# Kernel optimization log

Measured on AMD Instinct MI355X. Metric: run time of the kernel, lower is better.

The kernel has to match this reference:

```python
import jax, jax.numpy as jnp
import numpy as np

GROUPS = 4      # DySample groups (default)
DSTATE = 16     # SSM state size
BN_EPS = 1e-5


def grid_sample_border(img, grid):
    # img: (N, C, H, W); grid: (N, Ho, Wo, 2), xy order, [-1, 1], align_corners=False,
    # padding_mode='border' (coords clamped before bilinear interp).
    N, C, H, W = img.shape
    x = jnp.clip((grid[..., 0] + 1.0) * (W * 0.5) - 0.5, 0.0, W - 1.0)
    y = jnp.clip((grid[..., 1] + 1.0) * (H * 0.5) - 0.5, 0.0, H - 1.0)
    x0 = jnp.floor(x); y0 = jnp.floor(y)
    wx = (x - x0)[:, None]; wy = (y - y0)[:, None]          # (N,1,Ho,Wo)
    x0i = x0.astype(jnp.int32); y0i = y0.astype(jnp.int32)
    x1i = jnp.minimum(x0i + 1, W - 1); y1i = jnp.minimum(y0i + 1, H - 1)
    gat = jax.vmap(lambda im, yy, xx: im[:, yy, xx])        # (C,H,W),(Ho,Wo)->(C,Ho,Wo)
    v00 = gat(img, y0i, x0i); v01 = gat(img, y0i, x1i)
    v10 = gat(img, y1i, x0i); v11 = gat(img, y1i, x1i)
    return v00 * (1 - wx) * (1 - wy) + v01 * wx * (1 - wy) + v10 * (1 - wx) * wy + v11 * wx * wy


def dysample(x, off_w, off_b, scale):
    # DySample 'lp' style (ICCV'23), groups=4, no dyscope.
    B, C, H, W = x.shape
    s, g = scale, GROUPS
    conv = jnp.einsum('bchw,co->bohw', x, off_w) + off_b[None, :, None, None]  # (B, 2*g*s*s, H, W)
    hh = ((jnp.arange(s) - (s - 1) / 2.0) / s).astype(x.dtype)                 # subpixel init positions
    ip_x = jnp.broadcast_to(hh[None, None, :], (g, s, s))
    ip_y = jnp.broadcast_to(hh[None, :, None], (g, s, s))
    ip = jnp.stack([ip_x, ip_y])                                               # (2, g, s, s)
    off = conv.reshape(B, 2, g, s, s, H, W) * 0.25 + ip[None, :, :, :, :, None, None]
    cx = jnp.arange(W, dtype=x.dtype) + 0.5
    cy = jnp.arange(H, dtype=x.dtype) + 0.5
    gx = 2.0 * (cx + off[:, 0]) / W - 1.0                                      # (B,g,s,s,H,W)
    gy = 2.0 * (cy[:, None] + off[:, 1]) / H - 1.0
    # pixel_shuffle: (B,g,si,sj,H,W) -> (B,g,H,si,W,sj) -> (B,g,sH,sW)
    gx = gx.transpose(0, 1, 4, 2, 5, 3).reshape(B, g, s * H, s * W)
    gy = gy.transpose(0, 1, 4, 2, 5, 3).reshape(B, g, s * H, s * W)
    grid = jnp.stack([gx, gy], -1).reshape(B * g, s * H, s * W, 2)
    xg = x.reshape(B * g, C // g, H, W)
    return grid_sample_border(xg, grid).reshape(B, C, s * H, s * W)


def channel_ssm(x, in_w, in_b, xproj_w, dt_w, dt_b, A_log, Dp, out_w, out_b):
    # Channel-wise bidirectional selective scan (S6) over the channel axis, gating x.
    B, C, H, W = x.shape
    n = DSTATE
    s = x.mean((-2, -1))                            # (B, C) channel descriptor
    u = s[..., None] * in_w + in_b                  # (B, C, d)
    proj = u @ xproj_w                              # (B, C, 1 + 2n)
    dt_raw = proj[..., :1]
    Bs = proj[..., 1:1 + n]
    Cs = proj[..., 1 + n:]
    dt = jax.nn.softplus(dt_raw * dt_w + dt_b)      # (B, C, d)
    A = -jnp.exp(A_log)                             # (d, n)
    dA = jnp.exp(dt[..., None] * A)                 # (B, C, d, n)
    dBu = (dt * u)[..., None] * Bs[:, :, None, :]   # (B, C, d, n)

    def scan_dir(dA_, dBu_, Cs_):
        def step(h, inp):
            a, b, c = inp
            h = a * h + b                           # (B, d, n)
            return h, jnp.einsum('bdn,bn->bd', h, c)
        h0 = jnp.zeros((B, dA_.shape[2], n), x.dtype)
        _, ys = jax.lax.scan(step, h0, (jnp.swapaxes(dA_, 0, 1), jnp.swapaxes(dBu_, 0, 1), jnp.swapaxes(Cs_, 0, 1)))
        return jnp.swapaxes(ys, 0, 1)               # (B, C, d)

    y = scan_dir(dA, dBu, Cs)
    y = y + scan_dir(dA[:, ::-1], dBu[:, ::-1], Cs[:, ::-1])[:, ::-1]
    y = y + Dp * u
    gate = jax.nn.sigmoid(y @ out_w + out_b)        # (B, C)
    return x * gate[:, :, None, None]


def setup_inputs():
    key = jax.random.key(0)
    ks = jax.random.split(key, 24)
    f = jnp.float32
    rn = lambda k, shp, sc=1.0: jax.random.normal(k, shp, dtype=f) * sc
    B = 2
    inp = {}
    inp['c1'] = rn(ks[0], (B, 96, 128, 128))
    inp['c2'] = rn(ks[1], (B, 96, 64, 64))
    inp['c3'] = rn(ks[2], (B, 192, 32, 32))
    inp['c4'] = rn(ks[3], (B, 384, 16, 16))
    inp['mlp1_w'] = rn(ks[4], (96, 384), 0.05); inp['mlp1_b'] = jnp.zeros((384,), f)
    inp['mlp2_w'] = rn(ks[5], (96, 384), 0.05); inp['mlp2_b'] = jnp.zeros((384,), f)
    inp['mlp3_w'] = rn(ks[6], (192, 384), 0.05); inp['mlp3_b'] = jnp.zeros((384,), f)
    inp['mlp4_w'] = rn(ks[7], (384, 384), 0.05); inp['mlp4_b'] = jnp.zeros((384,), f)
    inp['up2_w'] = rn(ks[8], (384, 2 * 4 * 4), 0.001); inp['up2_b'] = jnp.zeros((2 * 4 * 4,), f)
    inp['up4_w'] = rn(ks[9], (384, 2 * 4 * 16), 0.001); inp['up4_b'] = jnp.zeros((2 * 4 * 16,), f)
    inp['up8_w'] = rn(ks[10], (384, 2 * 4 * 64), 0.001); inp['up8_b'] = jnp.zeros((2 * 4 * 64,), f)
    inp['ssm_in_w'] = rn(ks[11], (64,), 0.5); inp['ssm_in_b'] = rn(ks[12], (64,), 0.1)
    inp['ssm_xproj_w'] = rn(ks[13], (64, 1 + 2 * 16), 0.1)
    inp['ssm_dt_w'] = rn(ks[14], (64,), 0.1); inp['ssm_dt_b'] = jnp.full((64,), -2.0, f)
    inp['ssm_A_log'] = jnp.log(jnp.broadcast_to(jnp.arange(1, 17, dtype=f), (64, 16)))
    inp['ssm_D'] = jnp.ones((64,), f)
    inp['ssm_out_w'] = rn(ks[15], (64,), 0.1); inp['ssm_out_b'] = jnp.zeros((), f)
    inp['fuse_w'] = rn(ks[16], (1536, 384), 0.02)
    inp['bn_g'] = jnp.ones((384,), f); inp['bn_b'] = jnp.zeros((384,), f)
    inp['bn_m'] = jnp.zeros((384,), f); inp['bn_v'] = jnp.ones((384,), f)
    inp['pred_w'] = rn(ks[17], (384, 6), 0.05); inp['pred_b'] = jnp.zeros((6,), f)
    inp['bird_w'] = rn(ks[18], (384, 2), 0.05); inp['bird_b'] = jnp.zeros((2,), f)
    return inp


def reference(c1, c2, c3, c4, mlp1_w, mlp1_b, mlp2_w, mlp2_b, mlp3_w, mlp3_b, mlp4_w, mlp4_b,
              up2_w, up2_b, up4_w, up4_b, up8_w, up8_b,
              ssm_in_w, ssm_in_b, ssm_xproj_w, ssm_dt_w, ssm_dt_b, ssm_A_log, ssm_D, ssm_out_w, ssm_out_b,
              fuse_w, bn_g, bn_b, bn_m, bn_v, pred_w, pred_b, bird_w, bird_b):
    proj = lambda c, w, b: jnp.einsum('bchw,ce->behw', c, w) + b[None, :, None, None]
    _c4 = dysample(proj(c4, mlp4_w, mlp4_b), up8_w, up8_b, 8)
    _c3 = dysample(proj(c3, mlp3_w, mlp3_b), up4_w, up4_b, 4)
    _c2 = dysample(proj(c2, mlp2_w, mlp2_b), up2_w, up2_b, 2)
    _c1 = proj(c1, mlp1_w, mlp1_b)
    cc = jnp.concatenate([_c4, _c3, _c2, _c1], axis=1)      # (B, 1536, 128, 128)
    cc = channel_ssm(cc, ssm_in_w, ssm_in_b, ssm_xproj_w, ssm_dt_w, ssm_dt_b, ssm_A_log, ssm_D, ssm_out_w, ssm_out_b)
    h = jnp.einsum('bchw,co->bohw', cc, fuse_w)             # 1x1 conv, no bias
    h = (h - bn_m[None, :, None, None]) * (bn_g / jnp.sqrt(bn_v + BN_EPS))[None, :, None, None] + bn_b[None, :, None, None]
    h = jax.nn.relu(h)                                      # dropout = identity (eval)
    out = jnp.einsum('bchw,co->bohw', h, pred_w) + pred_b[None, :, None, None]
    aux = jnp.einsum('bchw,co->bohw', h, bird_w) + bird_b[None, :, None, None]
    return (out, aux)
```

## Files before the change

kernel.cpp:

```cpp
#include <hip/hip_runtime.h>
#include <cstddef>

#define HWO 16384
#define CTOT 1536

typedef __attribute__((ext_vector_type(8))) short bf16x8;
typedef __attribute__((ext_vector_type(4))) float f32x4;

__device__ inline unsigned short f2bf(float x) {
  union { float f; unsigned u; } v; v.f = x;
  unsigned r = v.u + 0x7FFFu + ((v.u >> 16) & 1u);
  return (unsigned short)(r >> 16);
}
__device__ inline float bf2f(unsigned short h) {
  union { unsigned u; float f; } v; v.u = ((unsigned)h) << 16; return v.f;
}

struct __align__(16) Prm { unsigned short i00, i01, i10, i11; float wx, wy; };

struct SetupArgs {
  const float* W[7];
  unsigned short* T[7];
  int K[7], N[7], bstart[8];
  const float *bn_g, *bn_v, *bn_m, *bn_b;
  float *sc, *sh;
  const float* c1;
  float* mc1;
  const float* fw;
  unsigned short* fwt;
  int nTP;
};
__global__ __launch_bounds__(256) void setup_kernel(SetupArgs a) {
  int bid = blockIdx.x;
  if (bid < a.nTP) {
    int s = 0;
#pragma unroll
    for (int i = 1; i < 7; i++) if (bid >= a.bstart[i]) s = i;
    const int K = a.K[s], N = a.N[s];
    const int idx = (bid - a.bstart[s]) * 256 + threadIdx.x;
    if (idx >= K * N) return;
    const int k = idx / N, o = idx - k * N;
    a.T[s][(size_t)o * K + k] = f2bf(a.W[s][idx]);
    return;
  }
  bid -= a.nTP;
  if (bid < 2) {
    const int o = bid * 256 + threadIdx.x;
    if (o < 384) {
      const float sc = a.bn_g[o] * rsqrtf(a.bn_v[o] + 1e-5f);
      a.sc[o] = sc;
      a.sh[o] = a.bn_b[o] - a.bn_m[o] * sc;
    }
    return;
  }
  bid -= 2;
  if (bid < 192) {
    const float4* p = (const float4*)(a.c1 + (size_t)bid * HWO);
    float acc = 0.f;
    for (int i = threadIdx.x; i < HWO / 4; i += 256) {
      const float4 v = p[i];
      acc += (v.x + v.y) + (v.z + v.w);
    }
    for (int o = 32; o > 0; o >>= 1) acc += __shfl_down(acc, o, 64);
    __shared__ float red[4];
    if ((threadIdx.x & 63) == 0) red[threadIdx.x >> 6] = acc;
    __syncthreads();
    if (threadIdx.x == 0)
      a.mc1[bid] = (red[0] + red[1] + red[2] + red[3]) * (1.0f / HWO);
    return;
  }
  bid -= 192;
  const int tk = bid / 12, to = bid % 12;
  __shared__ float tile[32][33];
  const int rr0 = threadIdx.x >> 5, cch = threadIdx.x & 31;
#pragma unroll
  for (int rr = rr0; rr < 32; rr += 8)
    tile[rr][cch] = a.fw[(size_t)(tk * 32 + rr) * 384 + to * 32 + cch];
  __syncthreads();
#pragma unroll
  for (int rr = rr0; rr < 32; rr += 8)
    a.fwt[(size_t)(to * 32 + rr) * 1536 + tk * 32 + cch] = f2bf(tile[cch][rr]);
}

struct PSeg { const float* X; const unsigned short* Wt; const float* bias;
              unsigned short* Y; int P, K, blk0; };
struct PArgs { PSeg s[4]; };
__global__ __launch_bounds__(256) void proj_all(PArgs a) {
  int si = 0;
#pragma unroll
  for (int i = 1; i < 4; i++) if ((int)blockIdx.x >= a.s[i].blk0) si = i;
  const PSeg sg = a.s[si];
  const int rel = blockIdx.x - sg.blk0;
  const int pb = rel >> 1, ob = rel & 1;
  const int b = blockIdx.y;
  const int P = sg.P, K = sg.K;
  const int p0 = pb * 128;
  constexpr int LST = 40;
  __shared__ unsigned short Alds[128 * LST];
  __shared__ unsigned short Blds[192 * LST];
  const int tid = threadIdx.x;
  const int w = tid >> 6, lane = tid & 63;
  const int wm = w >> 1, wn = w & 1;
  const float* Xf = sg.X + (long)b * K * P;
  const unsigned short* Wt = sg.Wt;
  f32x4 acc[24];
#pragma unroll
  for (int i = 0; i < 24; i++) acc[i] = (f32x4){0.f, 0.f, 0.f, 0.f};
  const int lr = lane & 15, lk = (lane >> 4) * 8;

  for (int kc = 0; kc < K; kc += 32) {
#pragma unroll
    for (int it = 0; it < 4; it++) {
      const int idx = tid + it * 256;
      const int k = idx >> 5, pg = (idx & 31) * 4;
      const float4 v = *(const float4*)(Xf + (long)(kc + k) * P + p0 + pg);
      Alds[(pg + 0) * LST + k] = f2bf(v.x);
      Alds[(pg + 1) * LST + k] = f2bf(v.y);
      Alds[(pg + 2) * LST + k] = f2bf(v.z);
      Alds[(pg + 3) * LST + k] = f2bf(v.w);
    }
#pragma unroll
    for (int it = 0; it < 3; it++) {
      const int idx = tid + it * 256;
      const int r = idx >> 2, ck = (idx & 3) * 8;
      *(uint4*)&Blds[r * LST + ck] =
          *(const uint4*)(Wt + (long)(ob * 192 + r) * K + kc + ck);
    }
    __syncthreads();
    bf16x8 af[4];
#pragma unroll
    for (int mt = 0; mt < 4; mt++)
      af[mt] = *(const bf16x8*)&Alds[((wm * 4 + mt) * 16 + lr) * LST + lk];
#pragma unroll
    for (int ot = 0; ot < 6; ot++) {
      const bf16x8 bfr = *(const bf16x8*)&Blds[((wn * 6 + ot) * 16 + lr) * LST + lk];
#pragma unroll
      for (int mt = 0; mt < 4; mt++)
        acc[mt * 6 + ot] = __builtin_amdgcn_mfma_f32_16x16x32_bf16(
            af[mt], bfr, acc[mt * 6 + ot], 0, 0, 0);
    }
    __syncthreads();
  }
  const int r0 = (lane >> 4) * 4;
#pragma unroll
  for (int mt = 0; mt < 4; mt++) {
#pragma unroll
    for (int ot = 0; ot < 6; ot++) {
      const int o = ob * 192 + (wn * 6 + ot) * 16 + lr;
      const float bv = sg.bias[o];
      const f32x4 r = acc[mt * 6 + ot];
#pragma unroll
      for (int jj = 0; jj < 4; jj++) {
        const long row = p0 + (wm * 4 + mt) * 16 + r0 + jj;
        sg.Y[((long)b * P + row) * 384 + o] = f2bf(r[jj] + bv);
      }
    }
  }
}

struct OSeg { const unsigned short* X; const unsigned short* Wt;
              const float* bias; float* Y; int P, N, obn, blk0; };
struct OArgs { OSeg s[3]; };
__global__ __launch_bounds__(256) void offs_all(OArgs a) {
  int si = 0;
#pragma unroll
  for (int i = 1; i < 3; i++) if ((int)blockIdx.x >= a.s[i].blk0) si = i;
  const OSeg sg = a.s[si];
  const int rel = blockIdx.x - sg.blk0;
  const int pb = rel / sg.obn, ob = rel - pb * sg.obn;
  const int b = blockIdx.y;
  const int P = sg.P, N = sg.N;
  const int p0 = pb * 128, o0 = ob * 128;
  constexpr int LST = 40;
  __shared__ unsigned short Alds[128 * LST];
  __shared__ unsigned short Blds[128 * LST];
  const int tid = threadIdx.x;
  const int w = tid >> 6, lane = tid & 63;
  const int wm = w >> 1, wn = w & 1;
  const unsigned short* Xb = sg.X + (long)b * P * 384;
  f32x4 acc[16];
#pragma unroll
  for (int i = 0; i < 16; i++) acc[i] = (f32x4){0.f, 0.f, 0.f, 0.f};
  const int lr = lane & 15, lk = (lane >> 4) * 8;

  for (int kc = 0; kc < 384; kc += 32) {
#pragma unroll
    for (int it = 0; it < 2; it++) {
      const int idx = tid + it * 256;
      const int r = idx >> 2, ck = (idx & 3) * 8;
      *(uint4*)&Alds[r * LST + ck] =
          *(const uint4*)(Xb + (long)(p0 + r) * 384 + kc + ck);
    }
#pragma unroll
    for (int it = 0; it < 2; it++) {
      const int idx = tid + it * 256;
      const int r = idx >> 2, ck = (idx & 3) * 8;
      uint4 v = {0u, 0u, 0u, 0u};
      if (o0 + r < N)
        v = *(const uint4*)(sg.Wt + (long)(o0 + r) * 384 + kc + ck);
      *(uint4*)&Blds[r * LST + ck] = v;
    }
    __syncthreads();
    bf16x8 af[4];
#pragma unroll
    for (int mt = 0; mt < 4; mt++)
      af[mt] = *(const bf16x8*)&Alds[((wm * 4 + mt) * 16 + lr) * LST + lk];
#pragma unroll
    for (int ot = 0; ot < 4; ot++) {
      const bf16x8 bfr = *(const bf16x8*)&Blds[((wn * 4 + ot) * 16 + lr) * LST + lk];
#pragma unroll
      for (int mt = 0; mt < 4; mt++)
        acc[mt * 4 + ot] = __builtin_amdgcn_mfma_f32_16x16x32_bf16(
            af[mt], bfr, acc[mt * 4 + ot], 0, 0, 0);
    }
    __syncthreads();
  }
  const int r0 = (lane >> 4) * 4;
#pragma unroll
  for (int mt = 0; mt < 4; mt++) {
#pragma unroll
    for (int ot = 0; ot < 4; ot++) {
      const int o = o0 + (wn * 4 + ot) * 16 + lr;
      if (o < N) {
        const float bv = sg.bias[o];
        const f32x4 r = acc[mt * 4 + ot];
#pragma unroll
        for (int jj = 0; jj < 4; jj++) {
          const long row = p0 + (wm * 4 + mt) * 16 + r0 + jj;
          sg.Y[((long)b * P + row) * N + o] = r[jj] + bv;
        }
      }
    }
  }
}

__global__ __launch_bounds__(256) void pm_kernel(
    const float* __restrict__ bo4, const float* __restrict__ bo3,
    const float* __restrict__ bo2,
    const unsigned short* __restrict__ bp4, const unsigned short* __restrict__ bp3,
    const unsigned short* __restrict__ bp2,
    Prm* __restrict__ prm, float* __restrict__ part) {
  const int gp = blockIdx.y, b = blockIdx.z;
  const int lvl = gp >> 2, g = gp & 3;
  const float* bo; int ls, H, offC;
  const unsigned short* bpL; int HWs_;
  if (lvl == 0)      { bo = bo4; ls = 3; H = 16; offC = 512; bpL = bp4; HWs_ = 256; }
  else if (lvl == 1) { bo = bo3; ls = 2; H = 32; offC = 128; bpL = bp3; HWs_ = 1024; }
  else               { bo = bo2; ls = 1; H = 64; offC = 32;  bpL = bp2; HWs_ = 4096; }
  const int s = 1 << ls, ss = s * s, W = H;
  const int tid = threadIdx.x;
  __shared__ Prm Plds[512];

#pragma unroll
  for (int ii = 0; ii < 2; ii++) {
    const int li = tid + ii * 256;
    const int p = blockIdx.x * 512 + li;
    const int yo = p >> 7, xo = p & 127;
    const int h = yo >> ls, i = yo & (s - 1);
    const int w = xo >> ls, j = xo & (s - 1);
    const int sp = h * W + w;
    const float* offp = bo + ((size_t)b * (W * H) + sp) * offC;
    const float cx = offp[g * ss + i * s + j];
    const float cy = offp[(4 + g) * ss + i * s + j];
    const float inv_s = 1.0f / (float)s;
    const float offx = cx * 0.25f + ((float)j - (s - 1) * 0.5f) * inv_s;
    const float offy = cy * 0.25f + ((float)i - (s - 1) * 0.5f) * inv_s;
    float xf = fminf(fmaxf((float)w + offx, 0.0f), (float)(W - 1));
    float yf = fminf(fmaxf((float)h + offy, 0.0f), (float)(H - 1));
    const float x0f = floorf(xf), y0f = floorf(yf);
    const int x0 = (int)x0f, y0 = (int)y0f;
    const int x1 = min(x0 + 1, W - 1), y1 = min(y0 + 1, H - 1);
    Prm pr;
    pr.i00 = (unsigned short)(y0 * W + x0);
    pr.i01 = (unsigned short)(y0 * W + x1);
    pr.i10 = (unsigned short)(y1 * W + x0);
    pr.i11 = (unsigned short)(y1 * W + x1);
    pr.wx = xf - x0f;
    pr.wy = yf - y0f;
    prm[((size_t)b * 12 + gp) * HWO + p] = pr;
    Plds[li] = pr;
  }
  __syncthreads();

  const int chunk = tid % 12, pl = tid / 12;
  float acc[8];
#pragma unroll
  for (int j = 0; j < 8; j++) acc[j] = 0.f;
  const unsigned short* qb = bpL + (size_t)b * HWs_ * 384 + g * 96 + chunk * 8;
  if (tid < 252) {
    for (int it = 0; it < 25; it++) {
      const int pli = it * 21 + pl;
      if (pli < 512) {
        const Prm pr = Plds[pli];
        const float wx = pr.wx, wy = pr.wy;
        const float w00 = (1.f - wx) * (1.f - wy), w01 = wx * (1.f - wy);
        const float w10 = (1.f - wx) * wy, w11 = wx * wy;
        const uint4 v00 = *(const uint4*)(qb + (size_t)pr.i00 * 384);
        const uint4 v01 = *(const uint4*)(qb + (size_t)pr.i01 * 384);
        const uint4 v10 = *(const uint4*)(qb + (size_t)pr.i10 * 384);
        const uint4 v11 = *(const uint4*)(qb + (size_t)pr.i11 * 384);
        const unsigned short* s00 = (const unsigned short*)&v00;
        const unsigned short* s01 = (const unsigned short*)&v01;
        const unsigned short* s10 = (const unsigned short*)&v10;
        const unsigned short* s11 = (const unsigned short*)&v11;
#pragma unroll
        for (int j = 0; j < 8; j++)
          acc[j] += w00 * bf2f(s00[j]) + w01 * bf2f(s01[j]) +
                    w10 * bf2f(s10[j]) + w11 * bf2f(s11[j]);
      }
    }
  }
  __shared__ float red[12][8][22];
  if (tid < 252) {
#pragma unroll
    for (int j = 0; j < 8; j++) red[chunk][j][pl] = acc[j];
  }
  __syncthreads();
  if (tid < 96) {
    float sum = 0.f;
#pragma unroll
    for (int l = 0; l < 21; l++) sum += red[tid >> 3][tid & 7][l];
    part[((size_t)blockIdx.x * 2 + b) * 1152 + gp * 96 + tid] = sum;
  }
}

__global__ __launch_bounds__(64) void ssm_prep(
    const float* __restrict__ part, const float* __restrict__ mc1,
    const float* __restrict__ mlp1_w, const float* __restrict__ mlp1_b,
    const float* __restrict__ in_w, const float* __restrict__ in_b,
    const float* __restrict__ xproj_w, const float* __restrict__ dt_w,
    const float* __restrict__ dt_b, float* __restrict__ u_out,
    float2* __restrict__ dtdu_out, float* __restrict__ Bs_out,
    float* __restrict__ Cs_out) {
  const int bc = blockIdx.x;
  const int b = bc / 1536, c = bc - b * 1536;
  const int d = threadIdx.x;
  float sv;
  if (c < 1152) {
    float a = (d < 32) ? part[((size_t)d * 2 + b) * 1152 + c] : 0.f;
    a += __shfl_xor(a, 1, 64);  a += __shfl_xor(a, 2, 64);
    a += __shfl_xor(a, 4, 64);  a += __shfl_xor(a, 8, 64);
    a += __shfl_xor(a, 16, 64); a += __shfl_xor(a, 32, 64);
    sv = a * (1.0f / HWO);
  } else {
    const int c2 = c - 1152;
    float a = mc1[b * 96 + d] * mlp1_w[d * 384 + c2];
    if (d < 32) a += mc1[b * 96 + 64 + d] * mlp1_w[(64 + d) * 384 + c2];
    a += __shfl_xor(a, 1, 64);  a += __shfl_xor(a, 2, 64);
    a += __shfl_xor(a, 4, 64);  a += __shfl_xor(a, 8, 64);
    a += __shfl_xor(a, 16, 64); a += __shfl_xor(a, 32, 64);
    sv = a + mlp1_b[c2];
  }
  const float u = sv * in_w[d] + in_b[d];
  __shared__ float ush[64];
  __shared__ float proj[33];
  ush[d] = u;
  __syncthreads();
  if (d < 33) {
    float acc = 0.f;
    for (int k = 0; k < 64; k++) acc = fmaf(ush[k], xproj_w[k * 33 + d], acc);
    proj[d] = acc;
  }
  __syncthreads();
  float dtv = proj[0] * dt_w[d] + dt_b[d];
  dtv = (dtv > 20.0f) ? dtv : log1pf(__expf(dtv));
  u_out[(size_t)bc * 64 + d] = u;
  dtdu_out[(size_t)bc * 64 + d] = make_float2(dtv, dtv * u);
  if (d < 16) {
    Bs_out[(size_t)bc * 16 + d] = proj[1 + d];
    Cs_out[(size_t)bc * 16 + d] = proj[17 + d];
  }
}

__global__ __launch_bounds__(256) void ssm_scan_par(
    const float2* __restrict__ dtdu, const float* __restrict__ Bs,
    const float* __restrict__ Cs, const float* __restrict__ A_log,
    float* __restrict__ y) {
  const int d = blockIdx.x, dir = blockIdx.y, b = blockIdx.z;
  const int t = threadIdx.x;
  const int j = t >> 4, n = t & 15;
  const float A = -__expf(A_log[d * 16 + n]);
  const int s0 = j * 96;
  const int c0 = dir ? (1535 - s0) : s0;
  const int step = dir ? -1 : 1;
  const float2* dbase = dtdu + (size_t)b * 1536 * 64 + (size_t)c0 * 64 + d;
  const float* bbase = Bs + (size_t)b * 1536 * 16 + (size_t)c0 * 16 + n;
  const float* cbase = Cs + (size_t)b * 1536 * 16 + (size_t)c0 * 16 + n;
  const long dstep = (long)step * 64;
  const long bstep = (long)step * 16;

  float Ap = 1.f, Bp = 0.f;
  {
    const float2* dp = dbase;
    const float* bp = bbase;
    float2 td = *dp;
    float Bv = *bp;
    for (int i = 0; i < 96; i++) {
      const float2 tdc = td;
      const float Bc = Bv;
      dp += dstep; bp += bstep;
      if (i + 1 < 96) { td = *dp; Bv = *bp; }
      const float a = __expf(tdc.x * A);
      Bp = fmaf(a, Bp, tdc.y * Bc);
      Ap *= a;
    }
  }
  __shared__ float sA[16][16], sB[16][16];
  sA[j][n] = Ap;
  sB[j][n] = Bp;
  __syncthreads();
  float H = 0.f;
  for (int jj = 0; jj < j; jj++) H = fmaf(sA[jj][n], H, sB[jj][n]);

  float* yb = y + (size_t)(b * 2 + dir) * 1536 * 64;
  {
    const float2* dp = dbase;
    const float* bp = bbase;
    const float* cp = cbase;
    float2 td = *dp;
    float Bv = *bp;
    float Cv = *cp;
    float h = H;
    int c = c0;
    for (int i = 0; i < 96; i++) {
      const float2 tdc = td;
      const float Bc = Bv, Cc = Cv;
      dp += dstep; bp += bstep; cp += bstep;
      if (i + 1 < 96) { td = *dp; Bv = *bp; Cv = *cp; }
      const float a = __expf(tdc.x * A);
      h = fmaf(a, h, tdc.y * Bc);
      float pr = h * Cc;
      pr += __shfl_xor(pr, 1, 64);
      pr += __shfl_xor(pr, 2, 64);
      pr += __shfl_xor(pr, 4, 64);
      pr += __shfl_xor(pr, 8, 64);
      if (n == 0) yb[(size_t)c * 64 + d] = pr;
      c += step;
    }
  }
}

__global__ __launch_bounds__(64) void gate_kernel(
    const float* __restrict__ y, const float* __restrict__ u,
    const float* __restrict__ Dp, const float* __restrict__ out_w,
    const float* __restrict__ out_b, float* __restrict__ gate) {
  const int c = blockIdx.x, b = blockIdx.y, d = threadIdx.x;
  const size_t i = ((size_t)b * 1536 + c) * 64 + d;
  float yt = y[((size_t)(b * 2) * 1536 + c) * 64 + d]
           + y[((size_t)(b * 2 + 1) * 1536 + c) * 64 + d]
           + Dp[d] * u[i];
  float v = yt * out_w[d];
  for (int o = 32; o > 0; o >>= 1) v += __shfl_down(v, o, 64);
  if (d == 0) gate[b * 1536 + c] = 1.0f / (1.0f + __expf(-(v + out_b[0])));
}

__global__ __launch_bounds__(256) void gate_fold(
    const unsigned short* __restrict__ wtf, const float* __restrict__ gate,
    unsigned short* __restrict__ wg) {
  const int b = blockIdx.y;
  const int idx8 = blockIdx.x * 256 + threadIdx.x;
  const int o = idx8 / 192;
  const int k0 = (idx8 - o * 192) * 8;
  const size_t idx = (size_t)o * 1536 + k0;
  const uint4 v = *(const uint4*)(wtf + idx);
  const unsigned short* s = (const unsigned short*)&v;
  const float* g = gate + b * 1536 + k0;
  unsigned short r8[8];
#pragma unroll
  for (int j = 0; j < 8; j++) r8[j] = f2bf(bf2f(s[j]) * g[j]);
  *(uint4*)(wg + (size_t)b * 589824 + idx) = *(const uint4*)r8;
}

__global__ __launch_bounds__(1024, 4) void fuse_gemm(
    const unsigned short* __restrict__ bp4, const unsigned short* __restrict__ bp3,
    const unsigned short* __restrict__ bp2, const unsigned short* __restrict__ bp1,
    const Prm* __restrict__ prm, const unsigned short* __restrict__ wg,
    const float* __restrict__ ep_a, const float* __restrict__ ep_b,
    unsigned short* __restrict__ hbf) {
  constexpr int LST = 40;
  __shared__ unsigned short Alds[128 * LST];
  __shared__ unsigned short Blds[384 * LST];
  const int tid = threadIdx.x;
  const int w = tid >> 6, lane = tid & 63;
  const int wm = w >> 2, wn = w & 3;
  const int b = blockIdx.y;
  const int p0 = blockIdx.x * 128;
  const unsigned short* Wb = wg + (size_t)b * 589824;
  f32x4 acc[12];
#pragma unroll
  for (int i = 0; i < 12; i++) acc[i] = (f32x4){0.f, 0.f, 0.f, 0.f};
  const int lr = lane & 15, lk = (lane >> 4) * 8;
  const int ar = tid >> 2, ag = tid & 3;

  for (int gp = 0; gp < 12; ++gp) {
    const int lvl = gp >> 2;
    const unsigned short* bpL; int HWs_;
    if (lvl == 0)      { bpL = bp4; HWs_ = 256; }
    else if (lvl == 1) { bpL = bp3; HWs_ = 1024; }
    else               { bpL = bp2; HWs_ = 4096; }
    Prm pr; pr.i00 = pr.i01 = pr.i10 = pr.i11 = 0; pr.wx = pr.wy = 0.f;
    if (tid < 512) pr = prm[((size_t)b * 12 + gp) * HWO + p0 + ar];
    const float wx = pr.wx, wy = pr.wy;
    const float w00 = (1.f - wx) * (1.f - wy), w01 = wx * (1.f - wy);
    const float w10 = (1.f - wx) * wy, w11 = wx * wy;
#pragma unroll
    for (int t3 = 0; t3 < 3; ++t3) {
      const int kc = gp * 96 + t3 * 32;
      if (tid < 512) {
        const int colL = (gp & 3) * 96 + t3 * 32 + ag * 8;
        const unsigned short* qb = bpL + (size_t)b * HWs_ * 384 + colL;
        const uint4 v00 = *(const uint4*)(qb + (size_t)pr.i00 * 384);
        const uint4 v01 = *(const uint4*)(qb + (size_t)pr.i01 * 384);
        const uint4 v10 = *(const uint4*)(qb + (size_t)pr.i10 * 384);
        const uint4 v11 = *(const uint4*)(qb + (size_t)pr.i11 * 384);
        const unsigned short* s00 = (const unsigned short*)&v00;
        const unsigned short* s01 = (const unsigned short*)&v01;
        const unsigned short* s10 = (const unsigned short*)&v10;
        const unsigned short* s11 = (const unsigned short*)&v11;
        unsigned short r8[8];
#pragma unroll
        for (int jj = 0; jj < 8; jj++)
          r8[jj] = f2bf(w00 * bf2f(s00[jj]) + w01 * bf2f(s01[jj]) +
                        w10 * bf2f(s10[jj]) + w11 * bf2f(s11[jj]));
        *(uint4*)&Alds[ar * LST + ag * 8] = *(const uint4*)r8;
      }
      {
        const int r = tid >> 2, ck = (tid & 3) * 8;
        *(uint4*)&Blds[r * LST + ck] =
            *(const uint4*)(Wb + (size_t)r * 1536 + kc + ck);
      }
      if (tid >= 512) {
        const int idx = tid + 512;
        const int r = idx >> 2, ck = (idx & 3) * 8;
        *(uint4*)&Blds[r * LST + ck] =
            *(const uint4*)(Wb + (size_t)r * 1536 + kc + ck);
      }
      __syncthreads();
      bf16x8 af[2];
#pragma unroll
      for (int mt = 0; mt < 2; mt++)
        af[mt] = *(const bf16x8*)&Alds[((wm * 2 + mt) * 16 + lr) * LST + lk];
#pragma unroll
      for (int ot = 0; ot < 6; ot++) {
        const bf16x8 bfr = *(const bf16x8*)&Blds[((wn * 6 + ot) * 16 + lr) * LST + lk];
#pragma unroll
        for (int mt = 0; mt < 2; mt++)
          acc[mt * 6 + ot] = __builtin_amdgcn_mfma_f32_16x16x32_bf16(
              af[mt], bfr, acc[mt * 6 + ot], 0, 0, 0);
      }
      __syncthreads();
    }
  }
  for (int kc = 1152; kc < 1536; kc += 32) {
    if (tid < 512)
      *(uint4*)&Alds[ar * LST + ag * 8] =
          *(const uint4*)(bp1 + ((size_t)b * HWO + p0 + ar) * 384 +
                          (kc - 1152) + ag * 8);
    {
      const int r = tid >> 2, ck = (tid & 3) * 8;
      *(uint4*)&Blds[r * LST + ck] =
          *(const uint4*)(Wb + (size_t)r * 1536 + kc + ck);
    }
    if (tid >= 512) {
      const int idx = tid + 512;
      const int r = idx >> 2, ck = (idx & 3) * 8;
      *(uint4*)&Blds[r * LST + ck] =
          *(const uint4*)(Wb + (size_t)r * 1536 + kc + ck);
    }
    __syncthreads();
    bf16x8 af[2];
#pragma unroll
    for (int mt = 0; mt < 2; mt++)
      af[mt] = *(const bf16x8*)&Alds[((wm * 2 + mt) * 16 + lr) * LST + lk];
#pragma unroll
    for (int ot = 0; ot < 6; ot++) {
      const bf16x8 bfr = *(const bf16x8*)&Blds[((wn * 6 + ot) * 16 + lr) * LST + lk];
#pragma unroll
      for (int mt = 0; mt < 2; mt++)
        acc[mt * 6 + ot] = __builtin_amdgcn_mfma_f32_16x16x32_bf16(
            af[mt], bfr, acc[mt * 6 + ot], 0, 0, 0);
    }
    __syncthreads();
  }
  const int r0 = (lane >> 4) * 4;
#pragma unroll
  for (int mt = 0; mt < 2; mt++) {
#pragma unroll
    for (int ot = 0; ot < 6; ot++) {
      const int o = (wn * 6 + ot) * 16 + lr;
      const float sa = ep_a[o], sb = ep_b[o];
      const f32x4 r = acc[mt * 6 + ot];
#pragma unroll
      for (int jj = 0; jj < 4; jj++) {
        const size_t row = p0 + (wm * 2 + mt) * 16 + r0 + jj;
        hbf[((size_t)b * HWO + row) * 384 + o] =
            f2bf(fmaxf(fmaf(r[jj], sa, sb), 0.f));
      }
    }
  }
}

__global__ __launch_bounds__(256) void head_pm(
    const unsigned short* __restrict__ h,
    const float* __restrict__ pred_w, const float* __restrict__ pred_b,
    const float* __restrict__ bird_w, const float* __restrict__ bird_b,
    float* __restrict__ out) {
  const int idx = blockIdx.x * 256 + threadIdx.x;
  const int b = idx >> 14, p = idx & 16383;
  const unsigned short* hb = h + ((size_t)b * HWO + p) * 384;
  float a0 = pred_b[0], a1 = pred_b[1], a2 = pred_b[2];
  float a3 = pred_b[3], a4 = pred_b[4], a5 = pred_b[5];
  float a6 = bird_b[0], a7 = bird_b[1];
  for (int c8 = 0; c8 < 384; c8 += 8) {
    const uint4 v = *(const uint4*)(hb + c8);
    const unsigned short* sv = (const unsigned short*)&v;
#pragma unroll
    for (int jj = 0; jj < 8; jj++) {
      const int o = c8 + jj;
      const float hv = bf2f(sv[jj]);
      const float* pw = pred_w + o * 6;
      a0 = fmaf(hv, pw[0], a0);
      a1 = fmaf(hv, pw[1], a1);
      a2 = fmaf(hv, pw[2], a2);
      a3 = fmaf(hv, pw[3], a3);
      a4 = fmaf(hv, pw[4], a4);
      a5 = fmaf(hv, pw[5], a5);
      a6 = fmaf(hv, bird_w[o * 2 + 0], a6);
      a7 = fmaf(hv, bird_w[o * 2 + 1], a7);
    }
  }
  float* ob = out + (size_t)b * 6 * HWO + p;
  ob[0] = a0; ob[HWO] = a1; ob[2 * HWO] = a2;
  ob[3 * HWO] = a3; ob[4 * HWO] = a4; ob[5 * HWO] = a5;
  float* ab = out + (size_t)12 * HWO + (size_t)b * 2 * HWO + p;
  ab[0] = a6; ab[HWO] = a7;
}

extern "C" void kernel_launch(void* const* d_in, const int* in_sizes, int n_in,
                              void* d_out, int out_size, void* d_ws, size_t ws_size,
                              hipStream_t stream) {
  const float* c1      = (const float*)d_in[0];
  const float* c2      = (const float*)d_in[1];
  const float* c3      = (const float*)d_in[2];
  const float* c4      = (const float*)d_in[3];
  const float* mlp1_w  = (const float*)d_in[4];
  const float* mlp1_b  = (const float*)d_in[5];
  const float* mlp2_w  = (const float*)d_in[6];
  const float* mlp2_b  = (const float*)d_in[7];
  const float* mlp3_w  = (const float*)d_in[8];
  const float* mlp3_b  = (const float*)d_in[9];
  const float* mlp4_w  = (const float*)d_in[10];
  const float* mlp4_b  = (const float*)d_in[11];
  const float* up2_w   = (const float*)d_in[12];
  const float* up2_b   = (const float*)d_in[13];
  const float* up4_w   = (const float*)d_in[14];
  const float* up4_b   = (const float*)d_in[15];
  const float* up8_w   = (const float*)d_in[16];
  const float* up8_b   = (const float*)d_in[17];
  const float* ssm_in_w    = (const float*)d_in[18];
  const float* ssm_in_b    = (const float*)d_in[19];
  const float* ssm_xproj_w = (const float*)d_in[20];
  const float* ssm_dt_w    = (const float*)d_in[21];
  const float* ssm_dt_b    = (const float*)d_in[22];
  const float* ssm_A_log   = (const float*)d_in[23];
  const float* ssm_D       = (const float*)d_in[24];
  const float* ssm_out_w   = (const float*)d_in[25];
  const float* ssm_out_b   = (const float*)d_in[26];
  const float* fuse_w  = (const float*)d_in[27];
  const float* bn_g    = (const float*)d_in[28];
  const float* bn_b    = (const float*)d_in[29];
  const float* bn_m    = (const float*)d_in[30];
  const float* bn_v    = (const float*)d_in[31];
  const float* pred_w  = (const float*)d_in[32];
  const float* pred_b  = (const float*)d_in[33];
  const float* bird_w  = (const float*)d_in[34];
  const float* bird_b  = (const float*)d_in[35];
  float* outp = (float*)d_out;
  (void)in_sizes; (void)n_in; (void)out_size; (void)ws_size;

  float* ws = (float*)d_ws;
  size_t off = 0;
  auto alloc = [&](size_t n) { float* p = ws + off; off += n; return p; };
  unsigned short* bp1 = (unsigned short*)alloc(6291456);
  unsigned short* bp4 = (unsigned short*)alloc(98304);
  unsigned short* bp3 = (unsigned short*)alloc(393216);
  unsigned short* bp2 = (unsigned short*)alloc(1572864);
  float* bo4 = alloc(262144);
  float* bo3 = alloc(262144);
  float* bo2 = alloc(262144);
  Prm* prm = (Prm*)alloc(1572864);
  float* part = alloc(73728);
  float* mc1  = alloc(192);
  float* ub   = alloc(196608);
  float2* dtdu = (float2*)alloc(393216);
  float* Bsb  = alloc(49152);
  float* Csb  = alloc(49152);
  float* yb   = alloc(393216);
  float* gteb = alloc(3072);
  float* scb  = alloc(384);
  float* shb  = alloc(384);
  unsigned short* hbf = (unsigned short*)alloc(6291456);
  unsigned short* t1  = (unsigned short*)(ws + off);
  unsigned short* t2  = t1 + 36864;
  unsigned short* t3  = t2 + 36864;
  unsigned short* t4  = t3 + 73728;
  unsigned short* t8  = t4 + 147456;
  unsigned short* t4u = t8 + 196608;
  unsigned short* t2u = t4u + 49152;
  unsigned short* wtf = t2u + 12288;
  unsigned short* wg  = wtf + 589824;

  {
    SetupArgs sp;
    const float* Ws[7] = {mlp1_w, mlp2_w, mlp3_w, mlp4_w, up8_w, up4_w, up2_w};
    unsigned short* Ts[7] = {t1, t2, t3, t4, t8, t4u, t2u};
    const int Ks[7] = {96, 96, 192, 384, 384, 384, 384};
    const int Ns[7] = {384, 384, 384, 384, 512, 128, 32};
    int bs = 0;
    for (int i = 0; i < 7; i++) {
      sp.W[i] = Ws[i]; sp.T[i] = Ts[i]; sp.K[i] = Ks[i]; sp.N[i] = Ns[i];
      sp.bstart[i] = bs;
      bs += (Ks[i] * Ns[i] + 255) / 256;
    }
    sp.bstart[7] = bs;
    sp.nTP = bs;
    sp.bn_g = bn_g; sp.bn_v = bn_v; sp.bn_m = bn_m; sp.bn_b = bn_b;
    sp.sc = scb; sp.sh = shb;
    sp.c1 = c1; sp.mc1 = mc1;
    sp.fw = fuse_w; sp.fwt = wtf;
    hipLaunchKernelGGL(setup_kernel, dim3(bs + 2 + 192 + 576), dim3(256), 0, stream, sp);
  }

  {
    PArgs pa;
    pa.s[0] = {c4, t4, mlp4_b, bp4, 256, 384, 0};
    pa.s[1] = {c3, t3, mlp3_b, bp3, 1024, 192, 4};
    pa.s[2] = {c2, t2, mlp2_b, bp2, 4096, 96, 20};
    pa.s[3] = {c1, t1, mlp1_b, bp1, 16384, 96, 84};
    hipLaunchKernelGGL(proj_all, dim3(340, 2), dim3(256), 0, stream, pa);
  }
  {
    OArgs oa;
    oa.s[0] = {bp4, t8, up8_b, bo4, 256, 512, 4, 0};
    oa.s[1] = {bp3, t4u, up4_b, bo3, 1024, 128, 1, 8};
    oa.s[2] = {bp2, t2u, up2_b, bo2, 4096, 32, 1, 16};
    hipLaunchKernelGGL(offs_all, dim3(48, 2), dim3(256), 0, stream, oa);
  }
  hipLaunchKernelGGL(pm_kernel, dim3(32, 12, 2), dim3(256), 0, stream,
                     bo4, bo3, bo2, bp4, bp3, bp2, prm, part);
  hipLaunchKernelGGL(ssm_prep, dim3(3072), dim3(64), 0, stream,
                     part, mc1, mlp1_w, mlp1_b, ssm_in_w, ssm_in_b,
                     ssm_xproj_w, ssm_dt_w, ssm_dt_b, ub, dtdu, Bsb, Csb);
  hipLaunchKernelGGL(ssm_scan_par, dim3(64, 2, 2), dim3(256), 0, stream,
                     dtdu, Bsb, Csb, ssm_A_log, yb);
  hipLaunchKernelGGL(gate_kernel, dim3(1536, 2), dim3(64), 0, stream,
                     yb, ub, ssm_D, ssm_out_w, ssm_out_b, gteb);
  hipLaunchKernelGGL(gate_fold, dim3(288, 2), dim3(256), 0, stream, wtf, gteb, wg);
  hipLaunchKernelGGL(fuse_gemm, dim3(128, 2), dim3(1024), 0, stream,
                     bp4, bp3, bp2, bp1, prm, wg, scb, shb, hbf);
  hipLaunchKernelGGL(head_pm, dim3(128), dim3(256), 0, stream,
                     hbf, pred_w, pred_b, bird_w, bird_b, outp);
}
```

Before: 223.8 us.

## Fold gate into fuse GEMM B-load, widen proj blocks, split head reduction

Three separate changes. The gate_fold kernel is removed: fuse_gemm now stages the per-batch gate vector in shared memory and multiplies the bf16 weights by it while loading B tiles, which drops one launch and the gated-weight round trip through global memory. proj_all now uses 512-thread blocks that cover all 384 output channels at once, halving the block count and reusing each A tile across both former output halves; LDS row strides also shrink from 40 to 36. head_pm is replaced by head_v2, which gives each pixel 8 threads that reduce partial sums with shuffles, for more parallelism than the old one-thread-per-pixel loop.

```diff
diff --git a/kernel.cpp b/kernel.cpp
--- a/kernel.cpp
+++ b/kernel.cpp
@@ -85,22 +85,21 @@
 struct PSeg { const float* X; const unsigned short* Wt; const float* bias;
               unsigned short* Y; int P, K, blk0; };
 struct PArgs { PSeg s[4]; };
-__global__ __launch_bounds__(256) void proj_all(PArgs a) {
+__global__ __launch_bounds__(512) void proj_all(PArgs a) {
   int si = 0;
 #pragma unroll
   for (int i = 1; i < 4; i++) if ((int)blockIdx.x >= a.s[i].blk0) si = i;
   const PSeg sg = a.s[si];
-  const int rel = blockIdx.x - sg.blk0;
-  const int pb = rel >> 1, ob = rel & 1;
+  const int pb = blockIdx.x - sg.blk0;
   const int b = blockIdx.y;
   const int P = sg.P, K = sg.K;
   const int p0 = pb * 128;
-  constexpr int LST = 40;
+  constexpr int LST = 36;
   __shared__ unsigned short Alds[128 * LST];
-  __shared__ unsigned short Blds[192 * LST];
+  __shared__ unsigned short Blds[384 * LST];
   const int tid = threadIdx.x;
   const int w = tid >> 6, lane = tid & 63;
-  const int wm = w >> 1, wn = w & 1;
+  const int wm = w >> 2, wn = w & 3;
   const float* Xf = sg.X + (long)b * K * P;
   const unsigned short* Wt = sg.Wt;
   f32x4 acc[24];
@@ -110,8 +109,8 @@
 
   for (int kc = 0; kc < K; kc += 32) {
 #pragma unroll
-    for (int it = 0; it < 4; it++) {
-      const int idx = tid + it * 256;
+    for (int it = 0; it < 2; it++) {
+      const int idx = tid + it * 512;
       const int k = idx >> 5, pg = (idx & 31) * 4;
       const float4 v = *(const float4*)(Xf + (long)(kc + k) * P + p0 + pg);
       Alds[(pg + 0) * LST + k] = f2bf(v.x);
@@ -121,10 +120,10 @@
     }
 #pragma unroll
     for (int it = 0; it < 3; it++) {
-      const int idx = tid + it * 256;
+      const int idx = tid + it * 512;
       const int r = idx >> 2, ck = (idx & 3) * 8;
       *(uint4*)&Blds[r * LST + ck] =
-          *(const uint4*)(Wt + (long)(ob * 192 + r) * K + kc + ck);
+          *(const uint4*)(Wt + (long)r * K + kc + ck);
     }
     __syncthreads();
     bf16x8 af[4];
@@ -146,7 +145,7 @@
   for (int mt = 0; mt < 4; mt++) {
 #pragma unroll
     for (int ot = 0; ot < 6; ot++) {
-      const int o = ob * 192 + (wn * 6 + ot) * 16 + lr;
+      const int o = (wn * 6 + ot) * 16 + lr;
       const float bv = sg.bias[o];
       const f32x4 r = acc[mt * 6 + ot];
 #pragma unroll
@@ -454,43 +453,30 @@
   if (d == 0) gate[b * 1536 + c] = 1.0f / (1.0f + __expf(-(v + out_b[0])));
 }
 
-__global__ __launch_bounds__(256) void gate_fold(
-    const unsigned short* __restrict__ wtf, const float* __restrict__ gate,
-    unsigned short* __restrict__ wg) {
-  const int b = blockIdx.y;
-  const int idx8 = blockIdx.x * 256 + threadIdx.x;
-  const int o = idx8 / 192;
-  const int k0 = (idx8 - o * 192) * 8;
-  const size_t idx = (size_t)o * 1536 + k0;
-  const uint4 v = *(const uint4*)(wtf + idx);
-  const unsigned short* s = (const unsigned short*)&v;
-  const float* g = gate + b * 1536 + k0;
-  unsigned short r8[8];
-#pragma unroll
-  for (int j = 0; j < 8; j++) r8[j] = f2bf(bf2f(s[j]) * g[j]);
-  *(uint4*)(wg + (size_t)b * 589824 + idx) = *(const uint4*)r8;
-}
-
 __global__ __launch_bounds__(1024, 4) void fuse_gemm(
     const unsigned short* __restrict__ bp4, const unsigned short* __restrict__ bp3,
     const unsigned short* __restrict__ bp2, const unsigned short* __restrict__ bp1,
-    const Prm* __restrict__ prm, const unsigned short* __restrict__ wg,
+    const Prm* __restrict__ prm, const unsigned short* __restrict__ wtf,
+    const float* __restrict__ gate,
     const float* __restrict__ ep_a, const float* __restrict__ ep_b,
     unsigned short* __restrict__ hbf) {
-  constexpr int LST = 40;
+  constexpr int LST = 36;
   __shared__ unsigned short Alds[128 * LST];
   __shared__ unsigned short Blds[384 * LST];
+  __shared__ float gsh[1536];
   const int tid = threadIdx.x;
   const int w = tid >> 6, lane = tid & 63;
   const int wm = w >> 2, wn = w & 3;
   const int b = blockIdx.y;
   const int p0 = blockIdx.x * 128;
-  const unsigned short* Wb = wg + (size_t)b * 589824;
   f32x4 acc[12];
 #pragma unroll
   for (int i = 0; i < 12; i++) acc[i] = (f32x4){0.f, 0.f, 0.f, 0.f};
   const int lr = lane & 15, lk = (lane >> 4) * 8;
   const int ar = tid >> 2, ag = tid & 3;
+
+  for (int i = tid; i < 1536; i += 1024) gsh[i] = gate[b * 1536 + i];
+  __syncthreads();
 
   for (int gp = 0; gp < 12; ++gp) {
     const int lvl = gp >> 2;
@@ -526,14 +512,24 @@
       }
       {
         const int r = tid >> 2, ck = (tid & 3) * 8;
-        *(uint4*)&Blds[r * LST + ck] =
-            *(const uint4*)(Wb + (size_t)r * 1536 + kc + ck);
+        const uint4 v = *(const uint4*)(wtf + (size_t)r * 1536 + kc + ck);
+        const unsigned short* s = (const unsigned short*)&v;
+        unsigned short r8[8];
+#pragma unroll
+        for (int jj = 0; jj < 8; jj++)
+          r8[jj] = f2bf(bf2f(s[jj]) * gsh[kc + ck + jj]);
+        *(uint4*)&Blds[r * LST + ck] = *(const uint4*)r8;
       }
       if (tid >= 512) {
         const int idx = tid + 512;
         const int r = idx >> 2, ck = (idx & 3) * 8;
-        *(uint4*)&Blds[r * LST + ck] =
-            *(const uint4*)(Wb + (size_t)r * 1536 + kc + ck);
+        const uint4 v = *(const uint4*)(wtf + (size_t)r * 1536 + kc + ck);
+        const unsigned short* s = (const unsigned short*)&v;
+        unsigned short r8[8];
+#pragma unroll
+        for (int jj = 0; jj < 8; jj++)
+          r8[jj] = f2bf(bf2f(s[jj]) * gsh[kc + ck + jj]);
+        *(uint4*)&Blds[r * LST + ck] = *(const uint4*)r8;
       }
       __syncthreads();
       bf16x8 af[2];
@@ -558,14 +554,24 @@
                           (kc - 1152) + ag * 8);
     {
       const int r = tid >> 2, ck = (tid & 3) * 8;
-      *(uint4*)&Blds[r * LST + ck] =
-          *(const uint4*)(Wb + (size_t)r * 1536 + kc + ck);
+      const uint4 v = *(const uint4*)(wtf + (size_t)r * 1536 + kc + ck);
+      const unsigned short* s = (const unsigned short*)&v;
+      unsigned short r8[8];
+#pragma unroll
+      for (int jj = 0; jj < 8; jj++)
+        r8[jj] = f2bf(bf2f(s[jj]) * gsh[kc + ck + jj]);
+      *(uint4*)&Blds[r * LST + ck] = *(const uint4*)r8;
     }
     if (tid >= 512) {
       const int idx = tid + 512;
       const int r = idx >> 2, ck = (idx & 3) * 8;
-      *(uint4*)&Blds[r * LST + ck] =
-          *(const uint4*)(Wb + (size_t)r * 1536 + kc + ck);
+      const uint4 v = *(const uint4*)(wtf + (size_t)r * 1536 + kc + ck);
+      const unsigned short* s = (const unsigned short*)&v;
+      unsigned short r8[8];
+#pragma unroll
+      for (int jj = 0; jj < 8; jj++)
+        r8[jj] = f2bf(bf2f(s[jj]) * gsh[kc + ck + jj]);
+      *(uint4*)&Blds[r * LST + ck] = *(const uint4*)r8;
     }
     __syncthreads();
     bf16x8 af[2];
@@ -600,40 +606,53 @@
   }
 }
 
-__global__ __launch_bounds__(256) void head_pm(
+__global__ __launch_bounds__(256) void head_v2(
     const unsigned short* __restrict__ h,
     const float* __restrict__ pred_w, const float* __restrict__ pred_b,
     const float* __restrict__ bird_w, const float* __restrict__ bird_b,
     float* __restrict__ out) {
   const int idx = blockIdx.x * 256 + threadIdx.x;
-  const int b = idx >> 14, p = idx & 16383;
-  const unsigned short* hb = h + ((size_t)b * HWO + p) * 384;
-  float a0 = pred_b[0], a1 = pred_b[1], a2 = pred_b[2];
-  float a3 = pred_b[3], a4 = pred_b[4], a5 = pred_b[5];
-  float a6 = bird_b[0], a7 = bird_b[1];
-  for (int c8 = 0; c8 < 384; c8 += 8) {
-    const uint4 v = *(const uint4*)(hb + c8);
+  const int pg = idx >> 3, sub = idx & 7;
+  const int b = pg >> 14, p = pg & 16383;
+  const unsigned short* hb = h + ((size_t)b * HWO + p) * 384 + sub * 48;
+  float a[8];
+#pragma unroll
+  for (int k = 0; k < 8; k++) a[k] = 0.f;
+  for (int cg = 0; cg < 6; cg++) {
+    const uint4 v = *(const uint4*)(hb + cg * 8);
     const unsigned short* sv = (const unsigned short*)&v;
 #pragma unroll
     for (int jj = 0; jj < 8; jj++) {
-      const int o = c8 + jj;
+      const int o = sub * 48 + cg * 8 + jj;
       const float hv = bf2f(sv[jj]);
       const float* pw = pred_w + o * 6;
-      a0 = fmaf(hv, pw[0], a0);
-      a1 = fmaf(hv, pw[1], a1);
-      a2 = fmaf(hv, pw[2], a2);
-      a3 = fmaf(hv, pw[3], a3);
-      a4 = fmaf(hv, pw[4], a4);
-      a5 = fmaf(hv, pw[5], a5);
-      a6 = fmaf(hv, bird_w[o * 2 + 0], a6);
-      a7 = fmaf(hv, bird_w[o * 2 + 1], a7);
-    }
-  }
-  float* ob = out + (size_t)b * 6 * HWO + p;
-  ob[0] = a0; ob[HWO] = a1; ob[2 * HWO] = a2;
-  ob[3 * HWO] = a3; ob[4 * HWO] = a4; ob[5 * HWO] = a5;
-  float* ab = out + (size_t)12 * HWO + (size_t)b * 2 * HWO + p;
-  ab[0] = a6; ab[HWO] = a7;
+      a[0] = fmaf(hv, pw[0], a[0]);
+      a[1] = fmaf(hv, pw[1], a[1]);
+      a[2] = fmaf(hv, pw[2], a[2]);
+      a[3] = fmaf(hv, pw[3], a[3]);
+      a[4] = fmaf(hv, pw[4], a[4]);
+      a[5] = fmaf(hv, pw[5], a[5]);
+      a[6] = fmaf(hv, bird_w[o * 2 + 0], a[6]);
+      a[7] = fmaf(hv, bird_w[o * 2 + 1], a[7]);
+    }
+  }
+#pragma unroll
+  for (int st = 4; st > 0; st >>= 1) {
+#pragma unroll
+    for (int k = 0; k < 8; k++) a[k] += __shfl_down(a[k], st, 8);
+  }
+  if (sub == 0) {
+    float* ob = out + (size_t)b * 6 * HWO + p;
+    ob[0] = a[0] + pred_b[0];
+    ob[HWO] = a[1] + pred_b[1];
+    ob[2 * HWO] = a[2] + pred_b[2];
+    ob[3 * HWO] = a[3] + pred_b[3];
+    ob[4 * HWO] = a[4] + pred_b[4];
+    ob[5 * HWO] = a[5] + pred_b[5];
+    float* ab = out + (size_t)12 * HWO + (size_t)b * 2 * HWO + p;
+    ab[0] = a[6] + bird_b[0];
+    ab[HWO] = a[7] + bird_b[1];
+  }
 }
 
 extern "C" void kernel_launch(void* const* d_in, const int* in_sizes, int n_in,
@@ -708,7 +727,6 @@
   unsigned short* t4u = t8 + 196608;
   unsigned short* t2u = t4u + 49152;
   unsigned short* wtf = t2u + 12288;
-  unsigned short* wg  = wtf + 589824;
 
   {
     SetupArgs sp;
@@ -734,10 +752,10 @@
   {
     PArgs pa;
     pa.s[0] = {c4, t4, mlp4_b, bp4, 256, 384, 0};
-    pa.s[1] = {c3, t3, mlp3_b, bp3, 1024, 192, 4};
-    pa.s[2] = {c2, t2, mlp2_b, bp2, 4096, 96, 20};
-    pa.s[3] = {c1, t1, mlp1_b, bp1, 16384, 96, 84};
-    hipLaunchKernelGGL(proj_all, dim3(340, 2), dim3(256), 0, stream, pa);
+    pa.s[1] = {c3, t3, mlp3_b, bp3, 1024, 192, 2};
+    pa.s[2] = {c2, t2, mlp2_b, bp2, 4096, 96, 10};
+    pa.s[3] = {c1, t1, mlp1_b, bp1, 16384, 96, 42};
+    hipLaunchKernelGGL(proj_all, dim3(170, 2), dim3(512), 0, stream, pa);
   }
   {
     OArgs oa;
@@ -755,9 +773,8 @@
                      dtdu, Bsb, Csb, ssm_A_log, yb);
   hipLaunchKernelGGL(gate_kernel, dim3(1536, 2), dim3(64), 0, stream,
                      yb, ub, ssm_D, ssm_out_w, ssm_out_b, gteb);
-  hipLaunchKernelGGL(gate_fold, dim3(288, 2), dim3(256), 0, stream, wtf, gteb, wg);
   hipLaunchKernelGGL(fuse_gemm, dim3(128, 2), dim3(1024), 0, stream,
-                     bp4, bp3, bp2, bp1, prm, wg, scb, shb, hbf);
-  hipLaunchKernelGGL(head_pm, dim3(128), dim3(256), 0, stream,
+                     bp4, bp3, bp2, bp1, prm, wtf, gteb, scb, shb, hbf);
+  hipLaunchKernelGGL(head_v2, dim3(1024), dim3(256), 0, stream,
                      hbf, pred_w, pred_b, bird_w, bird_b, outp);
 }
```

Result: slower. 267.9 us (+19.7%).
